# Optimization experiments

Measured on AMD Instinct MI355X. Metric: run time of the kernel, lower is better.

## Reference

```python
import jax, jax.numpy as jnp
import numpy as np

DIM = 2048
N_HEADS = 32
N_KV = 8
HEAD_DIM = DIM // N_HEADS  # 64
N_REP = N_HEADS // N_KV    # 4
HALF = HEAD_DIM // 2
B = 2
T = 2048
THETA = 10000.0


def _rope(x, cos, sin):
    # x: [B,H,T,hd]; cos/sin: [T,HALF]. Pairs are interleaved (..., half, 2),
    # matching torch.view_as_complex on a (..., -1, 2) reshape.
    xr = x.reshape(x.shape[:-1] + (HALF, 2))
    x0, x1 = xr[..., 0], xr[..., 1]
    o0 = x0 * cos - x1 * sin
    o1 = x0 * sin + x1 * cos
    return jnp.stack([o0, o1], axis=-1).reshape(x.shape)


def setup_inputs() -> dict:
    key = jax.random.key(0)
    ks = jax.random.split(key, 6)
    x = jax.random.normal(ks[0], (B, T, DIM), dtype=jnp.float32)
    scale = 0.02
    wq = jax.random.normal(ks[1], (N_HEADS * HEAD_DIM, DIM), dtype=jnp.float32) * scale
    wk = jax.random.normal(ks[2], (N_KV * HEAD_DIM, DIM), dtype=jnp.float32) * scale
    wv = jax.random.normal(ks[3], (N_KV * HEAD_DIM, DIM), dtype=jnp.float32) * scale
    wo = jax.random.normal(ks[4], (DIM, DIM), dtype=jnp.float32) * scale
    # causal mask [1,1,T,T]
    mask = jnp.tril(jnp.ones((T, T), dtype=jnp.int32))[None, None]
    # RoPE tables (precompute_freqs_cis with theta=10000, scaling_factor=1.0)
    freqs = 1.0 / THETA ** (jnp.arange(HALF, dtype=jnp.float32) / HALF)
    angles = jnp.arange(2 * T, dtype=jnp.float32)[:, None] * freqs[None, :]
    return {"x": x, "mask": mask, "wq": wq, "wk": wk, "wv": wv, "wo": wo,
            "cos": jnp.cos(angles), "sin": jnp.sin(angles)}


def reference(x, mask, wq, wk, wv, wo, cos, sin):
    Bx, Tx, C = x.shape
    q = (x @ wq.T).reshape(Bx, Tx, N_HEADS, HEAD_DIM).transpose(0, 2, 1, 3)
    k = (x @ wk.T).reshape(Bx, Tx, N_KV, HEAD_DIM).transpose(0, 2, 1, 3)
    v = (x @ wv.T).reshape(Bx, Tx, N_KV, HEAD_DIM).transpose(0, 2, 1, 3)
    q = _rope(q, cos[:Tx], sin[:Tx])
    k = _rope(k, cos[:Tx], sin[:Tx])
    # GQA: head h attends to kv head h // N_REP (repeat_interleave semantics)
    qg = q.reshape(Bx, N_KV, N_REP, Tx, HEAD_DIM)
    att = jnp.einsum('bgrtd,bgsd->bgrts', qg, k) * (HEAD_DIM ** -0.5)
    m = mask[0, 0, :Tx, :Tx]  # broadcast over b,g,r
    att = jnp.where(m == 0, -jnp.inf, att)
    att = jax.nn.softmax(att, axis=-1)
    og = jnp.einsum('bgrts,bgsd->bgrtd', att, v)
    out = og.reshape(Bx, N_HEADS, Tx, HEAD_DIM).transpose(0, 2, 1, 3).reshape(Bx, Tx, C)
    return out @ wo.T
```

## Files before the change

kernel.cpp:

```cpp
#include <hip/hip_runtime.h>
#include <hip/hip_bf16.h>

typedef unsigned short u16;
typedef __attribute__((ext_vector_type(8))) short s16x8;
typedef __attribute__((ext_vector_type(4))) float f32x4;
typedef __attribute__((ext_vector_type(16))) float f32x16;
typedef __attribute__((ext_vector_type(4))) float f32x4v;
typedef __attribute__((ext_vector_type(4))) u16 u16x4;

#define DIM 2048
#define NH 32
#define NKV 8
#define HD 64
#define TT 2048
#define BB 2
#define MT (BB * TT)

__device__ __forceinline__ u16 f2bf(float f) {
    union { float f; unsigned u; } v; v.f = f;
    unsigned r = v.u + 0x7FFFu + ((v.u >> 16) & 1u);
    return (u16)(r >> 16);
}
__device__ __forceinline__ float bf2f(u16 h) {
    union { unsigned u; float f; } v; v.u = ((unsigned)h) << 16;
    return v.f;
}
__device__ __forceinline__ u16 cvtbf(float f) {
    __hip_bfloat16 hb = __float2bfloat16(f);
    return *reinterpret_cast<u16*>(&hb);
}
__device__ __forceinline__ void plane32swap(unsigned& a, unsigned& b) {
#if defined(__has_builtin)
#if __has_builtin(__builtin_amdgcn_permlane32_swap)
    auto t = __builtin_amdgcn_permlane32_swap((int)a, (int)b, false, false);
    a = (unsigned)t[0]; b = (unsigned)t[1];
#else
    asm volatile("v_permlane32_swap_b32 %0, %1" : "+v"(a), "+v"(b));
#endif
#else
    asm volatile("v_permlane32_swap_b32 %0, %1" : "+v"(a), "+v"(b));
#endif
}

__global__ void k_convert_all(const float* __restrict__ x, const float* __restrict__ wq,
                              const float* __restrict__ wk, const float* __restrict__ wv,
                              const float* __restrict__ wo,
                              u16* __restrict__ xb, u16* __restrict__ wqkv, u16* __restrict__ wob) {
    long i = (long)(blockIdx.x * 256 + threadIdx.x) * 4;
    const float* src; u16* dst; long o = i;
    if (o < 8388608L)            { src = x;  dst = xb; }
    else if ((o -= 8388608L) < 4194304L) { src = wq; dst = wqkv; }
    else if ((o -= 4194304L) < 1048576L) { src = wk; dst = wqkv + 4194304L; }
    else if ((o -= 1048576L) < 1048576L) { src = wv; dst = wqkv + 5242880L; }
    else { o -= 1048576L;          src = wo; dst = wob; }
    f32x4v f = *(const f32x4v*)(src + o);
    u16x4 out;
    #pragma unroll
    for (int e = 0; e < 4; ++e) out[e] = f2bf(f[e]);
    *(u16x4*)(dst + o) = out;
}

template<int BNF, bool OUTF32>
__global__ __launch_bounds__(512, 2) void k_gemm256(const u16* __restrict__ A, const u16* __restrict__ B,
                                                    void* __restrict__ C, int M, int N, int K) {
    constexpr int BN = 64 * BNF;
    constexpr int BH = 2048 * BNF;
    __shared__ u16 LDS[32768 + 4 * BH];
    const int nTn = N / BN;
    const int nwg = gridDim.x;
    const int wg = (blockIdx.x & 7) * (nwg >> 3) + (blockIdx.x >> 3);
    const int tm = wg / nTn, tn = wg % nTn;
    const int tid = threadIdx.x, wid = tid >> 6, lane = tid & 63;
    const int wr = wid >> 2, wc = wid & 3;
    const u16* Ab = A + (size_t)tm * 256 * K;
    const u16* Bb = B + (size_t)tn * BN * K;

    f32x4 acc[8][BNF] = {};
    s16x8 af[4], bfr[BNF];

    auto STAGE_A = [&](int buf, int kk, int kt) {
        u16* base = LDS + (buf * 2 + kk) * 8192;
        const u16* g = Ab + kt * 64 + kk * 32;
        #pragma unroll
        for (int i = 0; i < 2; ++i) {
            const int s = i * 512 + tid;
            const int row = s >> 2;
            const int cl = (s & 3) ^ ((row >> 1) & 3);
            __builtin_amdgcn_global_load_lds(
                (const __attribute__((address_space(1))) void*)(g + (size_t)row * K + cl * 8),
                (__attribute__((address_space(3))) void*)(base + (i * 512 + wid * 64) * 8), 16, 0, 0);
        }
    };
    auto STAGE_B = [&](int buf, int kk, int kt) {
        u16* base = LDS + 32768 + (buf * 2 + kk) * BH;
        const u16* g = Bb + kt * 64 + kk * 32;
        auto one = [&](int ch) {
            const int row = ch * 16 + (lane >> 2);
            const int cl = (lane & 3) ^ ((row >> 1) & 3);
            __builtin_amdgcn_global_load_lds(
                (const __attribute__((address_space(1))) void*)(g + (size_t)row * K + cl * 8),
                (__attribute__((address_space(3))) void*)(base + ch * 512), 16, 0, 0);
        };
        if constexpr (BNF == 4) { one(wid); one(8 + wid); }
        else if constexpr (BNF == 3) { one(wid); one(8 + (wid & 3)); }
        else { one(wid); }
    };
    auto LDA = [&](int buf, int kk, int mh) {
        const u16* base = LDS + (buf * 2 + kk) * 8192;
        #pragma unroll
        for (int m2 = 0; m2 < 4; ++m2) {
            const int row = wr * 128 + (mh * 4 + m2) * 16 + (lane & 15);
            const int cl = (lane >> 4) ^ ((row >> 1) & 3);
            af[m2] = *(const s16x8*)(base + row * 32 + cl * 8);
        }
    };
    auto LDB = [&](int buf, int kk) {
        const u16* base = LDS + 32768 + (buf * 2 + kk) * BH;
        #pragma unroll
        for (int n = 0; n < BNF; ++n) {
            const int row = wc * (16 * BNF) + n * 16 + (lane & 15);
            const int cl = (lane >> 4) ^ ((row >> 1) & 3);
            bfr[n] = *(const s16x8*)(base + row * 32 + cl * 8);
        }
    };
    auto MFMA16 = [&](int mh) {
        asm volatile("s_waitcnt lgkmcnt(0)" ::: "memory");
        __builtin_amdgcn_sched_barrier(0);
        __builtin_amdgcn_s_setprio(1);
        #pragma unroll
        for (int m2 = 0; m2 < 4; ++m2)
            #pragma unroll
            for (int n = 0; n < BNF; ++n)
                acc[mh * 4 + m2][n] =
                    __builtin_amdgcn_mfma_f32_16x16x32_bf16(af[m2], bfr[n], acc[mh * 4 + m2][n], 0, 0, 0);
        __builtin_amdgcn_s_setprio(0);
    };

    #define VMID() do { if constexpr (BNF == 2) asm volatile("s_waitcnt vmcnt(6)" ::: "memory"); \
                        else                    asm volatile("s_waitcnt vmcnt(8)" ::: "memory"); } while (0)
    #define VONE() do { if constexpr (BNF == 2) asm volatile("s_waitcnt vmcnt(3)" ::: "memory"); \
                        else                    asm volatile("s_waitcnt vmcnt(4)" ::: "memory"); } while (0)

    STAGE_A(0, 0, 0); STAGE_B(0, 0, 0);
    STAGE_A(0, 1, 0); STAGE_B(0, 1, 0);
    STAGE_A(1, 0, 1); STAGE_B(1, 0, 1);
    VMID();
    __builtin_amdgcn_s_barrier();

    const int NI = K >> 7;
    for (int it = 0; it < NI; ++it) {
        const bool last = (it == NI - 1);
        const int t1 = 2 * it + 1;
        LDA(0, 0, 0); LDB(0, 0);
        STAGE_A(1, 1, t1);
        __builtin_amdgcn_s_barrier();
        MFMA16(0);
        __builtin_amdgcn_s_barrier();

        LDA(0, 0, 1);
        STAGE_B(1, 1, t1);
        __builtin_amdgcn_s_barrier();
        MFMA16(1);
        VMID();
        __builtin_amdgcn_s_barrier();

        LDA(0, 1, 0); LDB(0, 1);
        if (!last) STAGE_A(0, 0, t1 + 1);
        __builtin_amdgcn_s_barrier();
        MFMA16(0);
        __builtin_amdgcn_s_barrier();

        LDA(0, 1, 1);
        if (!last) STAGE_B(0, 0, t1 + 1);
        __builtin_amdgcn_s_barrier();
        MFMA16(1);
        if (!last) VMID(); else VONE();
        __builtin_amdgcn_s_barrier();

        LDA(1, 0, 0); LDB(1, 0);
        if (!last) STAGE_A(0, 1, t1 + 1);
        __builtin_amdgcn_s_barrier();
        MFMA16(0);
        __builtin_amdgcn_s_barrier();

        LDA(1, 0, 1);
        if (!last) STAGE_B(0, 1, t1 + 1);
        __builtin_amdgcn_s_barrier();
        MFMA16(1);
        if (!last) VMID(); else asm volatile("s_waitcnt vmcnt(0)" ::: "memory");
        __builtin_amdgcn_s_barrier();

        LDA(1, 1, 0); LDB(1, 1);
        if (!last) STAGE_A(1, 0, t1 + 2);
        __builtin_amdgcn_s_barrier();
        MFMA16(0);
        __builtin_amdgcn_s_barrier();

        LDA(1, 1, 1);
        if (!last) STAGE_B(1, 0, t1 + 2);
        __builtin_amdgcn_s_barrier();
        MFMA16(1);
        if (!last) VMID();
        __builtin_amdgcn_s_barrier();
    }
    #undef VMID
    #undef VONE

    #pragma unroll
    for (int mf = 0; mf < 8; ++mf)
        #pragma unroll
        for (int n = 0; n < BNF; ++n)
            #pragma unroll
            for (int r = 0; r < 4; ++r) {
                const int row = tm * 256 + wr * 128 + mf * 16 + (lane >> 4) * 4 + r;
                const int col = tn * BN + wc * (16 * BNF) + n * 16 + (lane & 15);
                if (OUTF32) ((float*)C)[(size_t)row * N + col] = acc[mf][n][r];
                else        ((u16*)C)[(size_t)row * N + col] = f2bf(acc[mf][n][r]);
            }
}

__global__ void k_rope(const u16* __restrict__ qkv, const float* __restrict__ ct, const float* __restrict__ st,
                       u16* __restrict__ qo, u16* __restrict__ ko, u16* __restrict__ vo) {
    const int idx = blockIdx.x * 256 + threadIdx.x;
    const int c = idx % 384;
    const int bt = idx / 384;
    const int b = bt / TT, t = bt % TT;
    const s16x8 v = *(const s16x8*)(qkv + (size_t)bt * 3072 + c * 8);
    if (c < 320) {
        const bool isq = c < 256;
        const int base = isq ? c : c - 256;
        const int hh = base >> 3;
        const int di0 = (base & 7) * 4;
        const f32x4v cc = *(const f32x4v*)(ct + t * 32 + di0);
        const f32x4v ss = *(const f32x4v*)(st + t * 32 + di0);
        const float QS = isq ? 0.18033688f : 1.0f;
        s16x8 o;
        #pragma unroll
        for (int p = 0; p < 4; ++p) {
            const float x0 = bf2f((u16)v[2 * p]), x1 = bf2f((u16)v[2 * p + 1]);
            o[2 * p]     = (short)cvtbf((x0 * cc[p] - x1 * ss[p]) * QS);
            o[2 * p + 1] = (short)cvtbf((x0 * ss[p] + x1 * cc[p]) * QS);
        }
        u16* dst = isq ? (qo + ((size_t)(b * NH + hh) * TT + t) * HD + 2 * di0)
                       : (ko + ((size_t)(b * NKV + hh) * TT + t) * HD + 2 * di0);
        *(s16x8*)dst = o;
    } else {
        const int base = c - 320;
        const int hh = base >> 3;
        const int d0 = (base & 7) * 8;
        *(s16x8*)(vo + ((size_t)(b * NKV + hh) * TT + t) * HD + d0) = v;
    }
}

__global__ __launch_bounds__(256) void k_vtrans(const u16* __restrict__ vp, u16* __restrict__ vt) {
    __shared__ u16 tile[64][66];
    const int bg = blockIdx.x >> 5;
    const int t0 = (blockIdx.x & 31) * 64;
    const int tid = threadIdx.x;
    #pragma unroll
    for (int c = 0; c < 2; ++c) {
        const int idx = c * 256 + tid;
        const int tl = idx >> 3, dc = idx & 7;
        s16x8 v = *(const s16x8*)(vp + ((size_t)bg * TT + t0 + tl) * HD + dc * 8);
        *(s16x8*)(&tile[tl][dc * 8]) = v;
    }
    __syncthreads();
    #pragma unroll
    for (int c = 0; c < 2; ++c) {
        const int idx = c * 256 + tid;
        const int d = idx >> 3, tc = idx & 7;
        s16x8 v;
        #pragma unroll
        for (int e = 0; e < 8; ++e) v[e] = (short)tile[tc * 8 + e][d];
        *(s16x8*)(vt + ((size_t)bg * HD + d) * TT + t0 + tc * 8) = v;
    }
}

__global__ __launch_bounds__(512) void k_attn(const u16* __restrict__ Q, const u16* __restrict__ K,
                                              const u16* __restrict__ Vtg, u16* __restrict__ O) {
    const int bid = blockIdx.x;
    const int gq = bid >> 6;
    const int qt8 = (gq < 4) ? (7 - gq) : (gq - 4);
    const int bh = bid & 63;
    const int h = bh & 31;
    const int b = bh >> 5;
    const int g = h >> 2;
    __shared__ u16 Ks[2][4096];
    __shared__ u16 Vs[2][4096];
    const int tid = threadIdx.x, wave = tid >> 6, lane = tid & 63;
    const int c = lane & 31, hi = lane >> 5;
    const u16* Qg = Q + ((size_t)(b * NH + h) * TT + qt8 * 256) * HD;
    const u16* Kg = K + (size_t)(b * NKV + g) * TT * HD;
    const u16* Vg = Vtg + (size_t)(b * NKV + g) * HD * TT;

    s16x8 qa[4];
    #pragma unroll
    for (int kb = 0; kb < 4; ++kb)
        qa[kb] = *(const s16x8*)(Qg + (size_t)(wave * 32 + c) * HD + kb * 16 + hi * 8);

    const int rl = lane >> 3, ccl = lane & 7;
    const int sc = ccl ^ rl;
    auto stage = [&](int jj, int bi) {
        const int r = wave * 8 + rl;
        __builtin_amdgcn_global_load_lds(
            (const __attribute__((address_space(1))) void*)(Kg + ((size_t)(jj * 64 + r)) * HD + sc * 8),
            (__attribute__((address_space(3))) void*)(Ks[bi] + wave * 512), 16, 0, 0);
        __builtin_amdgcn_global_load_lds(
            (const __attribute__((address_space(1))) void*)(Vg + (size_t)r * TT + jj * 64 + sc * 8),
            (__attribute__((address_space(3))) void*)(Vs[bi] + wave * 512), 16, 0, 0);
    };

    f32x16 acc0 = {}, acc1 = {};
    float l = 0.f;
    const int ntiles = 4 * qt8 + 4;

    stage(0, 0);

    for (int j = 0; j < ntiles; ++j) {
        asm volatile("s_waitcnt vmcnt(0)" ::: "memory");
        __builtin_amdgcn_s_barrier();
        if (j + 1 < ntiles) stage(j + 1, (j + 1) & 1);
        const u16* Kb = Ks[j & 1];
        const u16* Vb = Vs[j & 1];

        f32x16 s0 = {}, s1 = {};
        __builtin_amdgcn_s_setprio(1);
        #pragma unroll
        for (int kb = 0; kb < 4; ++kb) {
            const s16x8 kf0 = *(const s16x8*)(Kb + c * 64 + (((2 * kb + hi) ^ ccl) * 8));
            const s16x8 kf1 = *(const s16x8*)(Kb + (32 + c) * 64 + (((2 * kb + hi) ^ ccl) * 8));
            s0 = __builtin_amdgcn_mfma_f32_32x32x16_bf16(kf0, qa[kb], s0, 0, 0, 0);
            s1 = __builtin_amdgcn_mfma_f32_32x32x16_bf16(kf1, qa[kb], s1, 0, 0, 0);
        }
        __builtin_amdgcn_s_setprio(0);

        if (j >= ntiles - 4) {
            const int kb64 = (j - (ntiles - 4)) * 64;
            if (kb64 + 63 > wave * 32) {
                const int q_loc = wave * 32 + c;
                #pragma unroll
                for (int r = 0; r < 16; ++r) {
                    const int crow = (r & 3) + 8 * (r >> 2) + 4 * hi;
                    if (kb64 + crow > q_loc)      s0[r] = -1e30f;
                    if (kb64 + 32 + crow > q_loc) s1[r] = -1e30f;
                }
            }
        }
        #pragma unroll
        for (int r = 0; r < 16; ++r) {
            s0[r] = __builtin_amdgcn_exp2f(s0[r]); l += s0[r];
            s1[r] = __builtin_amdgcn_exp2f(s1[r]); l += s1[r];
        }

        unsigned W0[8], W1[8];
        #pragma unroll
        for (int m = 0; m < 8; ++m) {
            float a0f = s0[2 * m], a1f = s0[2 * m + 1];
            float b0f = s1[2 * m], b1f = s1[2 * m + 1];
            asm("v_cvt_pk_bf16_f32 %0, %1, %2" : "=v"(W0[m]) : "v"(a0f), "v"(a1f));
            asm("v_cvt_pk_bf16_f32 %0, %1, %2" : "=v"(W1[m]) : "v"(b0f), "v"(b1f));
        }
        s16x8 pa[4];
        #pragma unroll
        for (int ks = 0; ks < 4; ++ks) {
            const int base = 4 * (ks & 1);
            unsigned a0 = (ks < 2) ? W0[base + 0] : W1[base + 0];
            unsigned b0 = (ks < 2) ? W0[base + 2] : W1[base + 2];
            unsigned a1 = (ks < 2) ? W0[base + 1] : W1[base + 1];
            unsigned b1 = (ks < 2) ? W0[base + 3] : W1[base + 3];
            plane32swap(a0, b0);
            plane32swap(a1, b1);
            union { unsigned w[4]; s16x8 v; } u;
            u.w[0] = a0; u.w[1] = a1; u.w[2] = b0; u.w[3] = b1;
            pa[ks] = u.v;
        }

        __builtin_amdgcn_s_setprio(1);
        #pragma unroll
        for (int kb = 0; kb < 4; ++kb) {
            const s16x8 vb0 = *(const s16x8*)(Vb + c * 64 + (((2 * kb + hi) ^ ccl) * 8));
            const s16x8 vb1 = *(const s16x8*)(Vb + (32 + c) * 64 + (((2 * kb + hi) ^ ccl) * 8));
            acc0 = __builtin_amdgcn_mfma_f32_32x32x16_bf16(pa[kb], vb0, acc0, 0, 0, 0);
            acc1 = __builtin_amdgcn_mfma_f32_32x32x16_bf16(pa[kb], vb1, acc1, 0, 0, 0);
        }
        __builtin_amdgcn_s_setprio(0);
    }

    l += __shfl_xor(l, 32, 64);
    const float inv = 1.0f / l;
    #pragma unroll
    for (int r = 0; r < 16; ++r) {
        const int crow = (r & 3) + 8 * (r >> 2) + 4 * hi;
        const float li = __shfl(inv, crow, 64);
        const size_t row = (size_t)b * TT + qt8 * 256 + wave * 32 + crow;
        O[row * DIM + h * 64 + c]      = cvtbf(acc0[r] * li);
        O[row * DIM + h * 64 + 32 + c] = cvtbf(acc1[r] * li);
    }
}

extern "C" void kernel_launch(void* const* d_in, const int* in_sizes, int n_in,
                              void* d_out, int out_size, void* d_ws, size_t ws_size,
                              hipStream_t stream) {
    const float* x  = (const float*)d_in[0];
    const float* wq = (const float*)d_in[2];
    const float* wk = (const float*)d_in[3];
    const float* wv = (const float*)d_in[4];
    const float* wo = (const float*)d_in[5];
    const float* ct = (const float*)d_in[6];
    const float* st = (const float*)d_in[7];
    char* ws = (char*)d_ws;
    u16* xb   = (u16*)(ws);
    u16* wqkv = (u16*)(ws + 16777216);
    u16* wob  = (u16*)(ws + 29360128);
    u16* qkv  = (u16*)(ws + 37748736);
    u16* kr   = (u16*)(ws + 62914560);
    u16* vp   = (u16*)(ws + 67108864);
    u16* qr   = xb;
    u16* ao   = qkv;
    u16* vt   = wqkv;

    k_convert_all<<<18432, 256, 0, stream>>>(x, wq, wk, wv, wo, xb, wqkv, wob);

    k_gemm256<3, false><<<(MT / 256) * (3072 / 192), 512, 0, stream>>>(xb, wqkv, qkv, MT, 3072, DIM);
    k_rope<<<MT * 384 / 256, 256, 0, stream>>>(qkv, ct, st, qr, kr, vp);
    k_vtrans<<<BB * NKV * (TT / 64), 256, 0, stream>>>(vp, vt);
    k_attn<<<8 * 64, 512, 0, stream>>>(qr, kr, vt, ao);
    k_gemm256<2, true><<<(MT / 256) * (DIM / 128), 512, 0, stream>>>(ao, wob, d_out, MT, DIM, DIM);
}
```

Baseline: 171.3 us.

## Read V directly from QKV in transpose kernel and reswizzle attention LDS layout

The rope kernel no longer copies V into a separate per-head buffer. The V transpose kernel now reads V straight from the fused QKV projection output, which removes one full write and read of V through global memory. Separately, the K/V LDS staging swizzle gains an extra XOR by wave index, and the fragment reads XOR by row group (plus an offset of 4 for the second half) to reduce LDS bank conflicts. The swizzle must stay consistent between the staged writes and the fragment reads, or attention results will be wrong.

```diff
diff --git a/kernel.cpp b/kernel.cpp
--- a/kernel.cpp
+++ b/kernel.cpp
@@ -220,48 +220,42 @@
 }
 
 __global__ void k_rope(const u16* __restrict__ qkv, const float* __restrict__ ct, const float* __restrict__ st,
-                       u16* __restrict__ qo, u16* __restrict__ ko, u16* __restrict__ vo) {
+                       u16* __restrict__ qo, u16* __restrict__ ko) {
     const int idx = blockIdx.x * 256 + threadIdx.x;
-    const int c = idx % 384;
-    const int bt = idx / 384;
+    const int c = idx % 320;
+    const int bt = idx / 320;
     const int b = bt / TT, t = bt % TT;
     const s16x8 v = *(const s16x8*)(qkv + (size_t)bt * 3072 + c * 8);
-    if (c < 320) {
-        const bool isq = c < 256;
-        const int base = isq ? c : c - 256;
-        const int hh = base >> 3;
-        const int di0 = (base & 7) * 4;
-        const f32x4v cc = *(const f32x4v*)(ct + t * 32 + di0);
-        const f32x4v ss = *(const f32x4v*)(st + t * 32 + di0);
-        const float QS = isq ? 0.18033688f : 1.0f;
-        s16x8 o;
-        #pragma unroll
-        for (int p = 0; p < 4; ++p) {
-            const float x0 = bf2f((u16)v[2 * p]), x1 = bf2f((u16)v[2 * p + 1]);
-            o[2 * p]     = (short)cvtbf((x0 * cc[p] - x1 * ss[p]) * QS);
-            o[2 * p + 1] = (short)cvtbf((x0 * ss[p] + x1 * cc[p]) * QS);
-        }
-        u16* dst = isq ? (qo + ((size_t)(b * NH + hh) * TT + t) * HD + 2 * di0)
-                       : (ko + ((size_t)(b * NKV + hh) * TT + t) * HD + 2 * di0);
-        *(s16x8*)dst = o;
-    } else {
-        const int base = c - 320;
-        const int hh = base >> 3;
-        const int d0 = (base & 7) * 8;
-        *(s16x8*)(vo + ((size_t)(b * NKV + hh) * TT + t) * HD + d0) = v;
-    }
-}
-
-__global__ __launch_bounds__(256) void k_vtrans(const u16* __restrict__ vp, u16* __restrict__ vt) {
+    const bool isq = c < 256;
+    const int base = isq ? c : c - 256;
+    const int hh = base >> 3;
+    const int di0 = (base & 7) * 4;
+    const f32x4v cc = *(const f32x4v*)(ct + t * 32 + di0);
+    const f32x4v ss = *(const f32x4v*)(st + t * 32 + di0);
+    const float QS = isq ? 0.18033688f : 1.0f;
+    s16x8 o;
+    #pragma unroll
+    for (int p = 0; p < 4; ++p) {
+        const float x0 = bf2f((u16)v[2 * p]), x1 = bf2f((u16)v[2 * p + 1]);
+        o[2 * p]     = (short)cvtbf((x0 * cc[p] - x1 * ss[p]) * QS);
+        o[2 * p + 1] = (short)cvtbf((x0 * ss[p] + x1 * cc[p]) * QS);
+    }
+    u16* dst = isq ? (qo + ((size_t)(b * NH + hh) * TT + t) * HD + 2 * di0)
+                   : (ko + ((size_t)(b * NKV + hh) * TT + t) * HD + 2 * di0);
+    *(s16x8*)dst = o;
+}
+
+__global__ __launch_bounds__(256) void k_vtrans(const u16* __restrict__ qkv, u16* __restrict__ vt) {
     __shared__ u16 tile[64][66];
     const int bg = blockIdx.x >> 5;
+    const int b = bg >> 3, g = bg & 7;
     const int t0 = (blockIdx.x & 31) * 64;
     const int tid = threadIdx.x;
     #pragma unroll
     for (int c = 0; c < 2; ++c) {
         const int idx = c * 256 + tid;
         const int tl = idx >> 3, dc = idx & 7;
-        s16x8 v = *(const s16x8*)(vp + ((size_t)bg * TT + t0 + tl) * HD + dc * 8);
+        s16x8 v = *(const s16x8*)(qkv + ((size_t)(b * TT + t0 + tl)) * 3072 + 2560 + g * 64 + dc * 8);
         *(s16x8*)(&tile[tl][dc * 8]) = v;
     }
     __syncthreads();
@@ -299,7 +293,8 @@
         qa[kb] = *(const s16x8*)(Qg + (size_t)(wave * 32 + c) * HD + kb * 16 + hi * 8);
 
     const int rl = lane >> 3, ccl = lane & 7;
-    const int sc = ccl ^ rl;
+    const int sc = ccl ^ rl ^ wave;
+    const int rsh = c >> 3;
     auto stage = [&](int jj, int bi) {
         const int r = wave * 8 + rl;
         __builtin_amdgcn_global_load_lds(
@@ -327,8 +322,9 @@
         __builtin_amdgcn_s_setprio(1);
         #pragma unroll
         for (int kb = 0; kb < 4; ++kb) {
-            const s16x8 kf0 = *(const s16x8*)(Kb + c * 64 + (((2 * kb + hi) ^ ccl) * 8));
-            const s16x8 kf1 = *(const s16x8*)(Kb + (32 + c) * 64 + (((2 * kb + hi) ^ ccl) * 8));
+            const int sl0 = (2 * kb + hi) ^ ccl ^ rsh;
+            const s16x8 kf0 = *(const s16x8*)(Kb + c * 64 + sl0 * 8);
+            const s16x8 kf1 = *(const s16x8*)(Kb + (32 + c) * 64 + (sl0 ^ 4) * 8);
             s0 = __builtin_amdgcn_mfma_f32_32x32x16_bf16(kf0, qa[kb], s0, 0, 0, 0);
             s1 = __builtin_amdgcn_mfma_f32_32x32x16_bf16(kf1, qa[kb], s1, 0, 0, 0);
         }
@@ -378,8 +374,9 @@
         __builtin_amdgcn_s_setprio(1);
         #pragma unroll
         for (int kb = 0; kb < 4; ++kb) {
-            const s16x8 vb0 = *(const s16x8*)(Vb + c * 64 + (((2 * kb + hi) ^ ccl) * 8));
-            const s16x8 vb1 = *(const s16x8*)(Vb + (32 + c) * 64 + (((2 * kb + hi) ^ ccl) * 8));
+            const int sl0 = (2 * kb + hi) ^ ccl ^ rsh;
+            const s16x8 vb0 = *(const s16x8*)(Vb + c * 64 + sl0 * 8);
+            const s16x8 vb1 = *(const s16x8*)(Vb + (32 + c) * 64 + (sl0 ^ 4) * 8);
             acc0 = __builtin_amdgcn_mfma_f32_32x32x16_bf16(pa[kb], vb0, acc0, 0, 0, 0);
             acc1 = __builtin_amdgcn_mfma_f32_32x32x16_bf16(pa[kb], vb1, acc1, 0, 0, 0);
         }
@@ -414,7 +411,6 @@
     u16* wob  = (u16*)(ws + 29360128);
     u16* qkv  = (u16*)(ws + 37748736);
     u16* kr   = (u16*)(ws + 62914560);
-    u16* vp   = (u16*)(ws + 67108864);
     u16* qr   = xb;
     u16* ao   = qkv;
     u16* vt   = wqkv;
@@ -422,8 +418,8 @@
     k_convert_all<<<18432, 256, 0, stream>>>(x, wq, wk, wv, wo, xb, wqkv, wob);
 
     k_gemm256<3, false><<<(MT / 256) * (3072 / 192), 512, 0, stream>>>(xb, wqkv, qkv, MT, 3072, DIM);
-    k_rope<<<MT * 384 / 256, 256, 0, stream>>>(qkv, ct, st, qr, kr, vp);
-    k_vtrans<<<BB * NKV * (TT / 64), 256, 0, stream>>>(vp, vt);
+    k_rope<<<MT * 320 / 256, 256, 0, stream>>>(qkv, ct, st, qr, kr);
+    k_vtrans<<<BB * NKV * (TT / 64), 256, 0, stream>>>(qkv, vt);
     k_attn<<<8 * 64, 512, 0, stream>>>(qr, kr, vt, ao);
     k_gemm256<2, true><<<(MT / 256) * (DIM / 128), 512, 0, stream>>>(ao, wob, d_out, MT, DIM, DIM);
 }
```

Result: no change. 168.7 us (-1.5%).
